# Optimization experiments

Measured on AMD Instinct MI355X. Metric: run time of the kernel, lower is better.

Reference implementation:

```python
import jax, jax.numpy as jnp
import numpy as np

N = 50000      # num nodes
IN = 256       # in_channels
H = 4          # heads
C = 64         # out_channels per head (concat=False -> out_dim = C)
HOPS = 3       # max_hops == num hops provided
E = 400000     # edges per hop
NEG_SLOPE = 0.2


def setup_inputs() -> dict:
    key = jax.random.key(0)
    ks = jax.random.split(key, 10)
    s_in = 1.0 / np.sqrt(IN)
    s_c = 1.0 / np.sqrt(C)
    return {
        "x": jax.random.normal(ks[0], (N, IN), jnp.float32),
        "ei0": jax.random.randint(ks[1], (2, E), 0, N, dtype=jnp.int32),
        "ei1": jax.random.randint(ks[2], (2, E), 0, N, dtype=jnp.int32),
        "ei2": jax.random.randint(ks[3], (2, E), 0, N, dtype=jnp.int32),
        # shared left/right projections (lin_l / lin_r, shared across hops)
        "W_l": jax.random.normal(ks[4], (IN, H * C), jnp.float32) * s_in,
        "b_l": jnp.zeros((H * C,), jnp.float32),
        "W_r": jax.random.normal(ks[5], (IN, H * C), jnp.float32) * s_in,
        "b_r": jnp.zeros((H * C,), jnp.float32),
        # hop-specific attention vectors and output biases
        "att": jax.random.normal(ks[6], (HOPS, H, C), jnp.float32) * s_c,
        "bias": jnp.zeros((HOPS, C), jnp.float32),
        # hop gate (single Linear since gate_hidden=None)
        "W_gate": jax.random.normal(ks[7], (IN, HOPS), jnp.float32) * s_in,
        "b_gate": jnp.zeros((HOPS,), jnp.float32),
    }


def _segment_softmax(logits, seg, n):
    # logits: [E, H], seg: [E] destination node ids
    m = jax.ops.segment_max(logits, seg, num_segments=n)          # [N, H]
    m = jnp.where(jnp.isfinite(m), m, 0.0)                        # empty segments -> 0
    ex = jnp.exp(logits - m[seg])
    s = jax.ops.segment_sum(ex, seg, num_segments=n)              # [N, H]
    return ex / (s[seg] + 1e-16)


def _gatv2_hop(x_l, x_r, edge_index, att_k, bias_k):
    # x_l, x_r: [N, H, C] shared projections; edge_index: [2, Ek]
    src, dst = edge_index[0], edge_index[1]
    s = jax.nn.leaky_relu(x_l[src] + x_r[dst], NEG_SLOPE)         # [Ek, H, C]
    alpha = jnp.einsum("ehc,hc->eh", s, att_k)                    # [Ek, H]
    alpha = _segment_softmax(alpha, dst, N)
    msg = jax.ops.segment_sum(x_l[src] * alpha[..., None], dst, num_segments=N)  # [N, H, C]
    return msg.mean(axis=1) + bias_k                              # concat=False -> head mean, [N, C]


def reference(x, ei0, ei1, ei2, W_l, b_l, W_r, b_r, att, bias, W_gate, b_gate):
    # shared projections computed once
    x_l = (x @ W_l + b_l).reshape(N, H, C)
    x_r = (x @ W_r + b_r).reshape(N, H, C)

    # hop 0 gets self-loops (add_self_loops=True); higher hops do not
    ar = jnp.arange(N, dtype=ei0.dtype)
    ei0_sl = jnp.concatenate([ei0, jnp.stack([ar, ar])], axis=1)
    edges = [ei0_sl, ei1, ei2]

    messages = jnp.stack(
        [_gatv2_hop(x_l, x_r, edges[k], att[k], bias[k]) for k in range(HOPS)],
        axis=1,
    )  # [N, HOPS, C]

    logits = x @ W_gate + b_gate                                  # [N, HOPS]
    weights = jax.nn.softmax(logits, axis=-1)
    out = jnp.einsum("nkc,nk->nc", messages, weights)             # [N, C]
    return out
```

## Files before the change

### kernel.cpp

```cpp
#include <hip/hip_runtime.h>
#include <math.h>

#define N_NODES 50000
#define IN_DIM 256
#define HEADS 4
#define CDIM 64
#define HC 256
#define HOPS 3
#define EDGES 400000
#define NEG_SLOPE 0.2f
#define SEG (EDGES + N_NODES)
#define TOT_E (3 * EDGES + N_NODES)
#define CAP 40

#define NB_GATE  ((N_NODES + 3) / 4)
#define NB_PACKW ((IN_DIM * 2 * HC) / 256)
#define NB_SCAT  ((TOT_E + 255) / 256)
#define GEMM_BX  ((N_NODES + 127) / 128)

typedef unsigned short ushort;
using short8  = __attribute__((ext_vector_type(8))) short;
using floatx4 = __attribute__((ext_vector_type(4))) float;
using f32x2   = __attribute__((ext_vector_type(2))) float;

__device__ __forceinline__ void decode_flat(int f, int& k, int& e)
{
    if (f < SEG)              { k = 0; e = f; }
    else if (f < SEG + EDGES) { k = 1; e = f - SEG; }
    else                      { k = 2; e = f - SEG - EDGES; }
}

__device__ __forceinline__ ushort f2bf(float f)
{
    unsigned u = __float_as_uint(f);
    unsigned r = u + 0x7fffu + ((u >> 16) & 1u);
    return (ushort)(r >> 16);
}

__device__ __forceinline__ f32x2 bf2x(unsigned u)
{
    f32x2 r;
    r.x = __uint_as_float(u << 16);
    r.y = __uint_as_float(u & 0xffff0000u);
    return r;
}

__device__ __forceinline__ f32x2 lrelu2(f32x2 v)
{
    return __builtin_elementwise_max(v, 0.2f * v);
}

__global__ __launch_bounds__(256) void prep(
    const float* __restrict__ X, const float* __restrict__ Wg,
    const float* __restrict__ bg, float* __restrict__ gw,
    ushort* __restrict__ Xb,
    const float* __restrict__ Wl, const float* __restrict__ Wr,
    ushort* __restrict__ WT,
    const int* __restrict__ ei0, const int* __restrict__ ei1,
    const int* __restrict__ ei2, int* __restrict__ cnt,
    int* __restrict__ bucket)
{
    const int blk = blockIdx.x;
    const int tid = threadIdx.x;

    if (blk < NB_GATE) {
        const int node = (blk * 256 + tid) >> 6;
        const int lane = tid & 63;
        if (node >= N_NODES) return;

        float4 xv = ((const float4*)(X + (size_t)node * IN_DIM))[lane];

        union { ushort s[4]; uint2 u; } o;
        o.s[0] = f2bf(xv.x); o.s[1] = f2bf(xv.y);
        o.s[2] = f2bf(xv.z); o.s[3] = f2bf(xv.w);
        ((uint2*)(Xb + (size_t)node * IN_DIM))[lane] = o.u;

        float a0 = 0.f, a1 = 0.f, a2 = 0.f;
        const int i0 = lane * 4;
        a0 += xv.x * Wg[(i0 + 0) * HOPS + 0]; a1 += xv.x * Wg[(i0 + 0) * HOPS + 1]; a2 += xv.x * Wg[(i0 + 0) * HOPS + 2];
        a0 += xv.y * Wg[(i0 + 1) * HOPS + 0]; a1 += xv.y * Wg[(i0 + 1) * HOPS + 1]; a2 += xv.y * Wg[(i0 + 1) * HOPS + 2];
        a0 += xv.z * Wg[(i0 + 2) * HOPS + 0]; a1 += xv.z * Wg[(i0 + 2) * HOPS + 1]; a2 += xv.z * Wg[(i0 + 2) * HOPS + 2];
        a0 += xv.w * Wg[(i0 + 3) * HOPS + 0]; a1 += xv.w * Wg[(i0 + 3) * HOPS + 1]; a2 += xv.w * Wg[(i0 + 3) * HOPS + 2];

        #pragma unroll
        for (int off = 32; off >= 1; off >>= 1) {
            a0 += __shfl_xor(a0, off);
            a1 += __shfl_xor(a1, off);
            a2 += __shfl_xor(a2, off);
        }
        if (lane == 0) {
            float l0 = a0 + bg[0], l1 = a1 + bg[1], l2 = a2 + bg[2];
            float m = fmaxf(l0, fmaxf(l1, l2));
            float e0 = expf(l0 - m), e1 = expf(l1 - m), e2 = expf(l2 - m);
            float inv = 1.f / (e0 + e1 + e2);
            gw[node * HOPS + 0] = e0 * inv;
            gw[node * HOPS + 1] = e1 * inv;
            gw[node * HOPS + 2] = e2 * inv;
        }
    } else if (blk < NB_GATE + NB_PACKW) {
        int id = (blk - NB_GATE) * 256 + tid;
        int n = id >> 8;
        int k = id & 255;
        float v = (n < HC) ? Wl[k * HC + n] : Wr[k * HC + (n - HC)];
        WT[(size_t)n * IN_DIM + k] = f2bf(v);
    } else {
        int f = (blk - NB_GATE - NB_PACKW) * 256 + tid;
        if (f >= TOT_E) return;
        int k, e; decode_flat(f, k, e);
        int s, d;
        if (k == 0 && e >= EDGES) { s = d = e - EDGES; }
        else {
            const int* ei = (k == 0) ? ei0 : (k == 1) ? ei1 : ei2;
            s = ei[e]; d = ei[EDGES + e];
        }
        int pos = atomicAdd(&cnt[k * N_NODES + d], 1);
        if (pos < CAP)
            bucket[((size_t)k * N_NODES + d) * CAP + pos] = s;
    }
}

#define TM 128
#define TN 128
#define TK 32
#define LDP 40

__global__ __launch_bounds__(256) void gemm_mfma(
    const ushort* __restrict__ Xb, const ushort* __restrict__ WT,
    const float* __restrict__ b_l, const float* __restrict__ b_r,
    ushort* __restrict__ xlb, ushort* __restrict__ xrb, int M)
{
    __shared__ ushort As[TM][LDP];
    __shared__ ushort Bs[TN][LDP];
    const int tid  = threadIdx.x;
    const int wave = tid >> 6, lane = tid & 63;
    const int row0 = blockIdx.x * TM;
    const int col0 = blockIdx.y * TN;
    const int wy = (wave >> 1) * 64, wx = (wave & 1) * 64;
    const int lrow = lane & 15, lk = (lane >> 4) * 8;

    floatx4 acc[4][4];
    #pragma unroll
    for (int i = 0; i < 4; i++)
        #pragma unroll
        for (int j = 0; j < 4; j++)
            acc[i][j] = (floatx4){0.f, 0.f, 0.f, 0.f};

    for (int k0 = 0; k0 < IN_DIM; k0 += TK) {
        #pragma unroll
        for (int j = 0; j < 2; j++) {
            int id = tid + 256 * j;
            int r  = id >> 2;
            int c  = (id & 3) * 8;
            int gr = row0 + r;
            uint4 v = make_uint4(0u, 0u, 0u, 0u);
            if (gr < M)
                v = *(const uint4*)(Xb + (size_t)gr * IN_DIM + k0 + c);
            *(uint4*)&As[r][c] = v;
        }
        #pragma unroll
        for (int j = 0; j < 2; j++) {
            int id = tid + 256 * j;
            int r  = id >> 2;
            int c  = (id & 3) * 8;
            *(uint4*)&Bs[r][c] =
                *(const uint4*)(WT + (size_t)(col0 + r) * IN_DIM + k0 + c);
        }
        __syncthreads();

        short8 af[4], bf[4];
        #pragma unroll
        for (int mi = 0; mi < 4; mi++)
            af[mi] = *(const short8*)&As[wy + mi * 16 + lrow][lk];
        #pragma unroll
        for (int ni = 0; ni < 4; ni++)
            bf[ni] = *(const short8*)&Bs[wx + ni * 16 + lrow][lk];

        #pragma unroll
        for (int mi = 0; mi < 4; mi++)
            #pragma unroll
            for (int ni = 0; ni < 4; ni++)
                acc[mi][ni] = __builtin_amdgcn_mfma_f32_16x16x32_bf16(
                    bf[ni], af[mi], acc[mi][ni], 0, 0, 0);
        __syncthreads();
    }

    const int csub = (lane >> 4) * 4;
    #pragma unroll
    for (int mi = 0; mi < 4; mi++) {
        int grow = row0 + wy + mi * 16 + lrow;
        if (grow < M) {
            #pragma unroll
            for (int ni = 0; ni < 4; ni++) {
                int gcol = col0 + wx + ni * 16 + csub;
                floatx4 v = acc[mi][ni];
                const bool left = (gcol < HC);
                const float4 b = left ? *(const float4*)(b_l + gcol)
                                      : *(const float4*)(b_r + gcol - HC);
                union { ushort s[4]; uint2 u; } o;
                o.s[0] = f2bf(v[0] + b.x);
                o.s[1] = f2bf(v[1] + b.y);
                o.s[2] = f2bf(v[2] + b.z);
                o.s[3] = f2bf(v[3] + b.w);
                ushort* dst = left ? (xlb + (size_t)grow * HC + gcol)
                                   : (xrb + (size_t)grow * HC + gcol - HC);
                *(uint2*)dst = o.u;
            }
        }
    }
}

__global__ __launch_bounds__(192) void node_all(
    const ushort* __restrict__ xlb, const ushort* __restrict__ xrb,
    const int* __restrict__ cnt, const int* __restrict__ bucket,
    const float* __restrict__ att, const float* __restrict__ gw,
    const float* __restrict__ bias, float* __restrict__ out)
{
    __shared__ float lds[HOPS][CDIM];
    const int n    = blockIdx.x;
    const int k    = threadIdx.x >> 6;
    const int lane = threadIdx.x & 63;
    const int half = lane >> 5;
    const int sub  = lane & 31;
    const unsigned laneoff = (unsigned)sub * 8;

    const int deg = min(cnt[k * N_NODES + n], CAP);
    const int* bk = bucket + ((size_t)k * N_NODES + n) * CAP;

    uint4 rq = *(const uint4*)(xrb + (size_t)n * HC + laneoff);
    f32x2 rr[4] = { bf2x(rq.x), bf2x(rq.y), bf2x(rq.z), bf2x(rq.w) };

    const float4 a0 = ((const float4*)(att + (size_t)k * HC))[sub * 2 + 0];
    const float4 a1 = ((const float4*)(att + (size_t)k * HC))[sub * 2 + 1];
    f32x2 w2[4] = { {a0.x, a0.y}, {a0.z, a0.w}, {a1.x, a1.y}, {a1.z, a1.w} };

    float denom = 0.f;
    f32x2 acc2[4] = { {0.f,0.f}, {0.f,0.f}, {0.f,0.f}, {0.f,0.f} };

    if (deg > 0) {
        const int degm1 = deg - 1;
        int myS = (lane < deg) ? bk[lane] : 0;
        const int npair = (deg + 1) >> 1;

        int s0 = __shfl(myS, min(half, degm1));
        uint4 q = *(const uint4*)(xlb + (unsigned)s0 * HC + laneoff);

        for (int j = 0; j < npair; j++) {
            int sn = __shfl(myS, min(2 * (j + 1) + half, degm1));
            uint4 qn = *(const uint4*)(xlb + (unsigned)sn * HC + laneoff);

            f32x2 f0 = bf2x(q.x), f1 = bf2x(q.y);
            f32x2 f2 = bf2x(q.z), f3 = bf2x(q.w);

            f32x2 pp = w2[0] * lrelu2(f0 + rr[0]);
            pp = __builtin_elementwise_fma(w2[1], lrelu2(f1 + rr[1]), pp);
            pp = __builtin_elementwise_fma(w2[2], lrelu2(f2 + rr[2]), pp);
            pp = __builtin_elementwise_fma(w2[3], lrelu2(f3 + rr[3]), pp);
            float p = pp.x + pp.y;

            p += __shfl_xor(p, 1);
            p += __shfl_xor(p, 2);
            p += __shfl_xor(p, 4);

            bool valid = (2 * j + half) < deg;
            float ex = valid ? __expf(p) : 0.f;
            denom += ex;
            f32x2 ex2 = { ex, ex };
            acc2[0] = __builtin_elementwise_fma(ex2, f0, acc2[0]);
            acc2[1] = __builtin_elementwise_fma(ex2, f1, acc2[1]);
            acc2[2] = __builtin_elementwise_fma(ex2, f2, acc2[2]);
            acc2[3] = __builtin_elementwise_fma(ex2, f3, acc2[3]);
            q = qn;
        }
    }

    denom += __shfl_xor(denom, 32);
    const float inv = (denom > 0.f) ? 1.f / denom : 0.f;
    const float g   = gw[n * HOPS + k];
    const float* bb = bias + (size_t)k * CDIM + (size_t)(sub & 7) * 8;

    #pragma unroll
    for (int i = 0; i < 4; i++) {
        acc2[i].x += __shfl_xor(acc2[i].x, 32);
        acc2[i].y += __shfl_xor(acc2[i].y, 32);
        acc2[i].x *= inv;
        acc2[i].y *= inv;
        acc2[i].x += __shfl_xor(acc2[i].x, 8);
        acc2[i].y += __shfl_xor(acc2[i].y, 8);
        acc2[i].x += __shfl_xor(acc2[i].x, 16);
        acc2[i].y += __shfl_xor(acc2[i].y, 16);
        if (lane < 8) {
            lds[k][lane * 8 + 2 * i]     = g * (acc2[i].x * 0.25f + bb[2 * i]);
            lds[k][lane * 8 + 2 * i + 1] = g * (acc2[i].y * 0.25f + bb[2 * i + 1]);
        }
    }
    __syncthreads();

    if (threadIdx.x < CDIM)
        out[(size_t)n * CDIM + threadIdx.x] =
            lds[0][threadIdx.x] + lds[1][threadIdx.x] + lds[2][threadIdx.x];
}

extern "C" void kernel_launch(void* const* d_in, const int* in_sizes, int n_in,
                              void* d_out, int out_size, void* d_ws, size_t ws_size,
                              hipStream_t stream)
{
    const float* x      = (const float*)d_in[0];
    const int*   ei0    = (const int*)d_in[1];
    const int*   ei1    = (const int*)d_in[2];
    const int*   ei2    = (const int*)d_in[3];
    const float* W_l    = (const float*)d_in[4];
    const float* b_l    = (const float*)d_in[5];
    const float* W_r    = (const float*)d_in[6];
    const float* b_r    = (const float*)d_in[7];
    const float* att    = (const float*)d_in[8];
    const float* bias   = (const float*)d_in[9];
    const float* W_gate = (const float*)d_in[10];
    const float* b_gate = (const float*)d_in[11];

    const size_t NHC = (size_t)N_NODES * HC;
    float* ws      = (float*)d_ws;
    float* gwbuf   = ws;
    int*   cnt     = (int*)(gwbuf + HOPS * N_NODES);
    int*   bucket  = cnt + HOPS * N_NODES;
    ushort* xlb    = (ushort*)(bucket + (size_t)HOPS * N_NODES * CAP);
    ushort* xrb    = xlb + NHC;
    ushort* Xb     = xrb + NHC;
    ushort* WT     = Xb + NHC;

    hipMemsetAsync(cnt, 0, (size_t)HOPS * N_NODES * sizeof(int), stream);

    prep<<<NB_GATE + NB_PACKW + NB_SCAT, 256, 0, stream>>>(
        x, W_gate, b_gate, gwbuf, Xb, W_l, W_r, WT,
        ei0, ei1, ei2, cnt, bucket);

    dim3 ggrid(GEMM_BX, 4);
    gemm_mfma<<<ggrid, 256, 0, stream>>>(Xb, WT, b_l, b_r, xlb, xrb, N_NODES);

    node_all<<<N_NODES, 192, 0, stream>>>(
        xlb, xrb, cnt, bucket, att, gwbuf, bias, (float*)d_out);
}
```

Before: 377.6 us.

## Restructure projection GEMM to 64-row blocks covering all 512 output columns

The projection GEMM now gives each block 64 rows and all 512 output columns (left and right projections), instead of 128x128 tiles on a 2D grid. The full 64x256 A tile is loaded into shared memory once, so each X row is read from global memory a single time rather than once per column tile. Only the B tile is streamed per K step. Each wave now holds a 64x128 accumulator, which raises register pressure; launch bounds request 2 blocks per CU. The GEMM is only one of three kernels, and the node aggregation kernel likely dominates total time.

```diff
diff --git a/kernel.cpp b/kernel.cpp
--- a/kernel.cpp
+++ b/kernel.cpp
@@ -16,7 +16,10 @@
 #define NB_GATE  ((N_NODES + 3) / 4)
 #define NB_PACKW ((IN_DIM * 2 * HC) / 256)
 #define NB_SCAT  ((TOT_E + 255) / 256)
-#define GEMM_BX  ((N_NODES + 127) / 128)
+#define GB 64
+#define GEMM_BLOCKS ((N_NODES + GB - 1) / GB)
+#define AP 264
+#define BP 40
 
 typedef unsigned short ushort;
 using short8  = __attribute__((ext_vector_type(8))) short;
@@ -119,91 +122,86 @@
     }
 }
 
-#define TM 128
-#define TN 128
-#define TK 32
-#define LDP 40
-
-__global__ __launch_bounds__(256) void gemm_mfma(
+__global__ __launch_bounds__(256, 2) void gemm_mfma(
     const ushort* __restrict__ Xb, const ushort* __restrict__ WT,
     const float* __restrict__ b_l, const float* __restrict__ b_r,
     ushort* __restrict__ xlb, ushort* __restrict__ xrb, int M)
 {
-    __shared__ ushort As[TM][LDP];
-    __shared__ ushort Bs[TN][LDP];
+    __shared__ ushort As[GB][AP];
+    __shared__ ushort Bs[512][BP];
     const int tid  = threadIdx.x;
     const int wave = tid >> 6, lane = tid & 63;
-    const int row0 = blockIdx.x * TM;
-    const int col0 = blockIdx.y * TN;
-    const int wy = (wave >> 1) * 64, wx = (wave & 1) * 64;
+    const int row0 = blockIdx.x * GB;
+    const int wx   = wave * 128;
     const int lrow = lane & 15, lk = (lane >> 4) * 8;
 
-    floatx4 acc[4][4];
+    #pragma unroll
+    for (int j = 0; j < 8; j++) {
+        int id = tid + 256 * j;
+        int r  = id >> 5;
+        int c  = (id & 31) * 8;
+        int gr = row0 + r;
+        uint4 v = make_uint4(0u, 0u, 0u, 0u);
+        if (gr < M)
+            v = *(const uint4*)(Xb + (size_t)gr * IN_DIM + c);
+        *(uint4*)&As[r][c] = v;
+    }
+
+    floatx4 acc[4][8];
     #pragma unroll
     for (int i = 0; i < 4; i++)
         #pragma unroll
-        for (int j = 0; j < 4; j++)
+        for (int j = 0; j < 8; j++)
             acc[i][j] = (floatx4){0.f, 0.f, 0.f, 0.f};
 
-    for (int k0 = 0; k0 < IN_DIM; k0 += TK) {
-        #pragma unroll
-        for (int j = 0; j < 2; j++) {
-            int id = tid + 256 * j;
-            int r  = id >> 2;
-            int c  = (id & 3) * 8;
-            int gr = row0 + r;
-            uint4 v = make_uint4(0u, 0u, 0u, 0u);
-            if (gr < M)
-                v = *(const uint4*)(Xb + (size_t)gr * IN_DIM + k0 + c);
-            *(uint4*)&As[r][c] = v;
-        }
-        #pragma unroll
-        for (int j = 0; j < 2; j++) {
+    for (int k0 = 0; k0 < IN_DIM; k0 += 32) {
+        __syncthreads();
+        #pragma unroll
+        for (int j = 0; j < 8; j++) {
             int id = tid + 256 * j;
             int r  = id >> 2;
             int c  = (id & 3) * 8;
             *(uint4*)&Bs[r][c] =
-                *(const uint4*)(WT + (size_t)(col0 + r) * IN_DIM + k0 + c);
+                *(const uint4*)(WT + (size_t)r * IN_DIM + k0 + c);
         }
         __syncthreads();
 
-        short8 af[4], bf[4];
+        short8 af[4], bf[8];
         #pragma unroll
         for (int mi = 0; mi < 4; mi++)
-            af[mi] = *(const short8*)&As[wy + mi * 16 + lrow][lk];
-        #pragma unroll
-        for (int ni = 0; ni < 4; ni++)
+            af[mi] = *(const short8*)&As[mi * 16 + lrow][k0 + lk];
+        #pragma unroll
+        for (int ni = 0; ni < 8; ni++)
             bf[ni] = *(const short8*)&Bs[wx + ni * 16 + lrow][lk];
 
         #pragma unroll
         for (int mi = 0; mi < 4; mi++)
             #pragma unroll
-            for (int ni = 0; ni < 4; ni++)
+            for (int ni = 0; ni < 8; ni++)
                 acc[mi][ni] = __builtin_amdgcn_mfma_f32_16x16x32_bf16(
                     bf[ni], af[mi], acc[mi][ni], 0, 0, 0);
-        __syncthreads();
     }
 
     const int csub = (lane >> 4) * 4;
+    const bool left = (wx < HC);
+    const float*  bvec = left ? b_l : b_r;
+    ushort*       obuf = left ? xlb : xrb;
+    const int     cbase = left ? wx : wx - HC;
     #pragma unroll
     for (int mi = 0; mi < 4; mi++) {
-        int grow = row0 + wy + mi * 16 + lrow;
+        int grow = row0 + mi * 16 + lrow;
         if (grow < M) {
             #pragma unroll
-            for (int ni = 0; ni < 4; ni++) {
-                int gcol = col0 + wx + ni * 16 + csub;
+            for (int ni = 0; ni < 8; ni++) {
+                int lc = cbase + ni * 16 + csub;
                 floatx4 v = acc[mi][ni];
-                const bool left = (gcol < HC);
-                const float4 b = left ? *(const float4*)(b_l + gcol)
-                                      : *(const float4*)(b_r + gcol - HC);
+                const float4 b = *(const float4*)(bvec + lc);
                 union { ushort s[4]; uint2 u; } o;
                 o.s[0] = f2bf(v[0] + b.x);
                 o.s[1] = f2bf(v[1] + b.y);
                 o.s[2] = f2bf(v[2] + b.z);
                 o.s[3] = f2bf(v[3] + b.w);
-                ushort* dst = left ? (xlb + (size_t)grow * HC + gcol)
-                                   : (xrb + (size_t)grow * HC + gcol - HC);
-                *(uint2*)dst = o.u;
+                *(uint2*)(obuf + (size_t)grow * HC + lc) = o.u;
             }
         }
     }
@@ -333,8 +331,7 @@
         x, W_gate, b_gate, gwbuf, Xb, W_l, W_r, WT,
         ei0, ei1, ei2, cnt, bucket);
 
-    dim3 ggrid(GEMM_BX, 4);
-    gemm_mfma<<<ggrid, 256, 0, stream>>>(Xb, WT, b_l, b_r, xlb, xrb, N_NODES);
+    gemm_mfma<<<GEMM_BLOCKS, 256, 0, stream>>>(Xb, WT, b_l, b_r, xlb, xrb, N_NODES);
 
     node_all<<<N_NODES, 192, 0, stream>>>(
         xlb, xrb, cnt, bucket, att, gwbuf, bias, (float*)d_out);
```

New measurement: 387.7 us. 2.7% more time.
